# Kernel tuning notes

Measured on AMD Instinct MI355X. Metric: run time of the kernel, lower is better.

## Reference

```python
import jax, jax.numpy as jnp
import numpy as np

L, H, D, DH, FF, V, MAXPOS, SENSE, ATT = 12, 12, 768, 64, 3072, 30522, 512, 64, 64


def layer_norm(x, g, b, eps=1e-12):
    mu = jnp.mean(x, axis=-1, keepdims=True)
    var = jnp.mean((x - mu) ** 2, axis=-1, keepdims=True)
    return (x - mu) / jnp.sqrt(var + eps) * g + b


def setup_inputs() -> dict:
    key = jax.random.key(0)
    ks = jax.random.split(key, 24)
    B, S = 32, 256
    s = 0.02
    inp = {
        "input_ids": jax.random.randint(ks[0], (B, S), 0, V, dtype=jnp.int32),
        "token_type_ids": jnp.zeros((B, S), jnp.int32),
        "attention_mask": jnp.ones((B, S), jnp.int32),
        "location": jax.random.randint(ks[1], (B,), 1, S, dtype=jnp.int32),
        "sense_emb": jax.random.normal(ks[2], (SENSE, D), jnp.float32),
        # embedding tables
        "word_emb": s * jax.random.normal(ks[3], (V, D), jnp.float32),
        "pos_emb": s * jax.random.normal(ks[4], (MAXPOS, D), jnp.float32),
        "type_emb": s * jax.random.normal(ks[5], (2, D), jnp.float32),
        "emb_ln_g": jnp.ones((D,), jnp.float32),
        "emb_ln_b": jnp.zeros((D,), jnp.float32),
        # stacked per-layer transformer weights [L, ...]
        "Wq": s * jax.random.normal(ks[6], (L, D, D), jnp.float32),
        "bq": jnp.zeros((L, D), jnp.float32),
        "Wk": s * jax.random.normal(ks[7], (L, D, D), jnp.float32),
        "bk": jnp.zeros((L, D), jnp.float32),
        "Wv": s * jax.random.normal(ks[8], (L, D, D), jnp.float32),
        "bv": jnp.zeros((L, D), jnp.float32),
        "Wo": s * jax.random.normal(ks[9], (L, D, D), jnp.float32),
        "bo": jnp.zeros((L, D), jnp.float32),
        "ln1_g": jnp.ones((L, D), jnp.float32),
        "ln1_b": jnp.zeros((L, D), jnp.float32),
        "W1": s * jax.random.normal(ks[10], (L, D, FF), jnp.float32),
        "b1": jnp.zeros((L, FF), jnp.float32),
        "W2": s * jax.random.normal(ks[11], (L, FF, D), jnp.float32),
        "b2": jnp.zeros((L, D), jnp.float32),
        "ln2_g": jnp.ones((L, D), jnp.float32),
        "ln2_b": jnp.zeros((L, D), jnp.float32),
        # SelfAttention(sense_num) projections, scale dim = 64
        "att_Wq": s * jax.random.normal(ks[12], (D, ATT), jnp.float32),
        "att_Wk": s * jax.random.normal(ks[13], (D, ATT), jnp.float32),
    }
    return inp


def bert_encode(input_ids, token_type_ids, attention_mask, word_emb, pos_emb,
                type_emb, emb_ln_g, emb_ln_b, Wq, bq, Wk, bk, Wv, bv, Wo, bo,
                ln1_g, ln1_b, W1, b1, W2, b2, ln2_g, ln2_b):
    B, S = input_ids.shape
    x = word_emb[input_ids] + pos_emb[:S][None, :, :] + type_emb[token_type_ids]
    x = layer_norm(x, emb_ln_g, emb_ln_b)
    # additive mask bias: [B,1,1,S]
    bias = (1.0 - attention_mask.astype(x.dtype))[:, None, None, :] * -10000.0
    scale = 1.0 / jnp.sqrt(jnp.asarray(DH, x.dtype))
    for l in range(L):
        q = (x @ Wq[l] + bq[l]).reshape(B, S, H, DH).transpose(0, 2, 1, 3)
        k = (x @ Wk[l] + bk[l]).reshape(B, S, H, DH).transpose(0, 2, 1, 3)
        v = (x @ Wv[l] + bv[l]).reshape(B, S, H, DH).transpose(0, 2, 1, 3)
        scores = jnp.einsum("bhqd,bhkd->bhqk", q, k) * scale + bias
        attn = jax.nn.softmax(scores, axis=-1)
        o = jnp.einsum("bhqk,bhkd->bhqd", attn, v)
        o = o.transpose(0, 2, 1, 3).reshape(B, S, D)
        x = layer_norm(x + o @ Wo[l] + bo[l], ln1_g[l], ln1_b[l])
        h = jax.nn.gelu(x @ W1[l] + b1[l], approximate=False)
        x = layer_norm(x + h @ W2[l] + b2[l], ln2_g[l], ln2_b[l])
    return x


def reference(input_ids, token_type_ids, attention_mask, location, sense_emb,
              word_emb, pos_emb, type_emb, emb_ln_g, emb_ln_b, Wq, bq, Wk, bk,
              Wv, bv, Wo, bo, ln1_g, ln1_b, W1, b1, W2, b2, ln2_g, ln2_b,
              att_Wq, att_Wk):
    last_layer = bert_encode(input_ids, token_type_ids, attention_mask,
                             word_emb, pos_emb, type_emb, emb_ln_g, emb_ln_b,
                             Wq, bq, Wk, bk, Wv, bv, Wo, bo, ln1_g, ln1_b,
                             W1, b1, W2, b2, ln2_g, ln2_b)
    B = last_layer.shape[0]
    # gather the pun-word embedding at `location[i]` per row  -> [B, D]
    pun = last_layer[jnp.arange(B), location]
    # SelfAttention(sense_num) with scale 64: scaled dot-product scores [B, SENSE]
    scores = (pun @ att_Wq) @ (sense_emb @ att_Wk).T / jnp.sqrt(jnp.asarray(ATT, pun.dtype))
    res = jax.nn.softmax(scores, axis=1)
    # fused top-2 (replaces the original per-scalar Python loop)
    _, idx = jax.lax.top_k(res, 2)
    return idx.astype(jnp.float32)
```

## Files before the change

### kernel.cpp

```cpp
#include <hip/hip_runtime.h>
#include <math.h>

typedef __attribute__((ext_vector_type(8))) short short8;
typedef __attribute__((ext_vector_type(8))) _Float16 half8;
typedef __attribute__((ext_vector_type(4))) float f32x4;

static constexpr int Lc = 12;
static constexpr int Hc = 12;
static constexpr int Dc = 768;
static constexpr int DHc = 64;
static constexpr int FFc = 3072;
static constexpr int SENSEc = 64;
static constexpr int ATTc = 64;
static constexpr int QS = 3 * Dc;
static constexpr int KPAD = 72;

__device__ __forceinline__ unsigned short f2h(float f) {
    _Float16 h = (_Float16)f;
    union { _Float16 h; unsigned short u; } c;
    c.h = h;
    return c.u;
}

__device__ __forceinline__ void load_lds16(const void* g, void* l) {
    __builtin_amdgcn_global_load_lds(
        (const __attribute__((address_space(1))) unsigned int*)g,
        (__attribute__((address_space(3))) unsigned int*)l, 16, 0, 0);
}

__device__ __forceinline__ float blockReduceSum256(float v, float* sred) {
#pragma unroll
    for (int off = 32; off > 0; off >>= 1) v += __shfl_down(v, off, 64);
    int lane = threadIdx.x & 63, wid = threadIdx.x >> 6;
    if (lane == 0) sred[wid] = v;
    __syncthreads();
    float total = sred[0] + sred[1] + sred[2] + sred[3];
    __syncthreads();
    return total;
}

__global__ __launch_bounds__(256) void embed_kernel(
    const int* __restrict__ ids, const int* __restrict__ tts,
    const float* __restrict__ we, const float* __restrict__ pe,
    const float* __restrict__ te, const float* __restrict__ g,
    const float* __restrict__ b, float* __restrict__ x,
    unsigned short* __restrict__ xh, int S)
{
    int tok = blockIdx.x, t = threadIdx.x;
    int ss = tok % S;
    int id = ids[tok], tt = tts[tok];
    __shared__ float sred[4];
    float v[3];
    float s = 0.f;
#pragma unroll
    for (int i = 0; i < 3; ++i) {
        int d = t + i * 256;
        v[i] = we[(size_t)id * Dc + d] + pe[(size_t)ss * Dc + d] + te[(size_t)tt * Dc + d];
        s += v[i];
    }
    float mu = blockReduceSum256(s, sred) * (1.f / Dc);
    float s2 = 0.f;
#pragma unroll
    for (int i = 0; i < 3; ++i) { v[i] -= mu; s2 += v[i] * v[i]; }
    float rstd = rsqrtf(blockReduceSum256(s2, sred) * (1.f / Dc) + 1e-12f);
    size_t ro = (size_t)tok * Dc;
#pragma unroll
    for (int i = 0; i < 3; ++i) {
        int d = t + i * 256;
        float val = v[i] * rstd * g[d] + b[d];
        x[ro + d] = val;
        xh[ro + d] = f2h(val);
    }
}

__global__ __launch_bounds__(256) void resln_kernel(
    float* __restrict__ x, const float* __restrict__ y,
    const float* __restrict__ g, const float* __restrict__ b,
    unsigned short* __restrict__ xh)
{
    int tok = blockIdx.x, t = threadIdx.x;
    __shared__ float sred[4];
    size_t ro = (size_t)tok * Dc;
    float v[3];
    float s = 0.f;
#pragma unroll
    for (int i = 0; i < 3; ++i) {
        int d = t + i * 256;
        v[i] = x[ro + d] + y[ro + d];
        s += v[i];
    }
    float mu = blockReduceSum256(s, sred) * (1.f / Dc);
    float s2 = 0.f;
#pragma unroll
    for (int i = 0; i < 3; ++i) { v[i] -= mu; s2 += v[i] * v[i]; }
    float rstd = rsqrtf(blockReduceSum256(s2, sred) * (1.f / Dc) + 1e-12f);
#pragma unroll
    for (int i = 0; i < 3; ++i) {
        int d = t + i * 256;
        float val = v[i] * rstd * g[d] + b[d];
        x[ro + d] = val;
        xh[ro + d] = f2h(val);
    }
}

__global__ __launch_bounds__(256) void convert_weights(
    const float* __restrict__ Wq, const float* __restrict__ Wk,
    const float* __restrict__ Wv, const float* __restrict__ Wo,
    const float* __restrict__ W1, const float* __restrict__ W2,
    unsigned short* __restrict__ qh, unsigned short* __restrict__ oh,
    unsigned short* __restrict__ h1, unsigned short* __restrict__ h2)
{
    int id = blockIdx.x;
    const float* src; unsigned short *dh; int Kd, Nd, tx, ty;
    if (id < 576) {
        int m = id / 144, tile = id % 144;
        src = (m == 0) ? Wq : (m == 1) ? Wk : (m == 2) ? Wv : Wo;
        if (m < 3) { dh = qh + (size_t)m * Dc * Dc; }
        else       { dh = oh; }
        Kd = Dc; Nd = Dc; tx = tile % 12; ty = tile / 12;
    } else if (id < 1152) {
        int tile = id - 576;
        src = W1; dh = h1; Kd = Dc; Nd = FFc; tx = tile % 48; ty = tile / 48;
    } else {
        int tile = id - 1152;
        src = W2; dh = h2; Kd = FFc; Nd = Dc; tx = tile % 12; ty = tile / 12;
    }
    int k0 = ty * 64, n0 = tx * 64;
    __shared__ float tileS[64][65];
    int t = threadIdx.x, c = t & 63, r0 = t >> 6;
#pragma unroll
    for (int i = 0; i < 16; ++i) {
        int kr = r0 + i * 4;
        tileS[kr][c] = src[(size_t)(k0 + kr) * Nd + n0 + c];
    }
    __syncthreads();
#pragma unroll
    for (int i = 0; i < 16; ++i) {
        int nr = r0 + i * 4;
        float v = tileS[c][nr];
        size_t idx = (size_t)(n0 + nr) * Kd + k0 + c;
        dh[idx] = f2h(v);
    }
}

__global__ __launch_bounds__(256) void biascat_kernel(
    const float* __restrict__ bq, const float* __restrict__ bk,
    const float* __restrict__ bv, float* __restrict__ out)
{
    int lyr = blockIdx.x, t = threadIdx.x;
    for (int j = t; j < QS; j += 256) {
        float v = (j < Dc) ? bq[lyr * Dc + j]
                : (j < 2 * Dc) ? bk[lyr * Dc + j - Dc]
                : bv[lyr * Dc + j - 2 * Dc];
        out[lyr * QS + j] = v;
    }
}

template <int MODE>
__global__ __launch_bounds__(256, 3) void mfma_gemm_f16(
    const unsigned short* __restrict__ Ah, const unsigned short* __restrict__ Bh,
    const float* __restrict__ bias, float* __restrict__ Cf,
    unsigned short* __restrict__ Ch, int M, int N, int K)
{
    __shared__ alignas(16) unsigned short Ash[128 * 64];
    __shared__ alignas(16) unsigned short Bsh[128 * 64];
    int t = threadIdx.x, w = t >> 6, l = t & 63;
    int m0 = blockIdx.y * 128, n0 = blockIdx.x * 128;
    int wm = (w >> 1) * 64, wn = (w & 1) * 64;
    int sw = (((l & 7) ^ (l >> 3)) << 3);
    size_t go = (size_t)(w * 8 + (l >> 3)) * K + sw;
    const unsigned short* gah = Ah + (size_t)m0 * K + go;
    const unsigned short* gbh = Bh + (size_t)n0 * K + go;
    int lo = w * 512 + l * 8;
    f32x4 acc[4][4];
#pragma unroll
    for (int i = 0; i < 4; ++i)
#pragma unroll
        for (int j = 0; j < 4; ++j) acc[i][j] = (f32x4)0.f;
    int fm = l & 15, grp = l >> 4;
    int axor = fm & 7;
    for (int k0 = 0; k0 < K; k0 += 64) {
        __syncthreads();
#pragma unroll
        for (int i = 0; i < 4; ++i) {
            size_t g = (size_t)(i * 32) * K + k0;
            int d = lo + i * 2048;
            load_lds16(gah + g, Ash + d);
            load_lds16(gbh + g, Bsh + d);
        }
        __syncthreads();
#pragma unroll
        for (int h = 0; h < 2; ++h) {
            int koff = (((h * 4 + grp) ^ axor) << 3);
            half8 fa[4], fb[4];
#pragma unroll
            for (int i = 0; i < 4; ++i) {
                int ra = (wm + i * 16 + fm) * 64 + koff;
                int rb = (wn + i * 16 + fm) * 64 + koff;
                fa[i] = *(const half8*)(Ash + ra);
                fb[i] = *(const half8*)(Bsh + rb);
            }
#pragma unroll
            for (int i = 0; i < 4; ++i)
#pragma unroll
                for (int j = 0; j < 4; ++j)
                    acc[i][j] = __builtin_amdgcn_mfma_f32_16x16x32_f16(
                        fa[i], fb[j], acc[i][j], 0, 0, 0);
        }
    }
    int col_l = l & 15, row_l = (l >> 4) * 4;
#pragma unroll
    for (int j = 0; j < 4; ++j) {
        int col = n0 + wn + j * 16 + col_l;
        float bcv = bias[col];
#pragma unroll
        for (int i = 0; i < 4; ++i) {
            int row = m0 + wm + i * 16 + row_l;
#pragma unroll
            for (int r = 0; r < 4; ++r) {
                float v = acc[i][j][r] + bcv;
                size_t idx = (size_t)(row + r) * N + col;
                if (MODE == 1) {
                    v = 0.5f * v * (1.f + erff(v * 0.70710678118654752f));
                    Ch[idx] = f2h(v);
                } else if (MODE == 2) {
                    Ch[idx] = f2h(v);
                } else {
                    Cf[idx] = v;
                }
            }
        }
    }
}

__global__ __launch_bounds__(256, 1) void attn_mfma(
    const unsigned short* __restrict__ qkv, const int* __restrict__ mask,
    unsigned short* __restrict__ aoh, int B, int S)
{
    int bh = blockIdx.x, b = bh / Hc, hd = bh % Hc;
    int t = threadIdx.x, w = t >> 6, l = t & 63;
    int grp = l >> 4, lc = l & 15;
    __shared__ alignas(16) unsigned short Ks[256 * 64];
    __shared__ alignas(16) unsigned short Vts[4][64 * KPAD];
    __shared__ alignas(16) unsigned short Pw[4][64 * KPAD];
    __shared__ float mb[256];
    size_t rowbase = (size_t)(b * S) * QS;

    mb[t] = (1.f - (float)mask[b * S + t]) * -10000.0f;

    for (int p = 0; p < 4; ++p) {
        int key = p * 64 + (t >> 2);
        int d0 = (t & 3) * 16;
        const unsigned short* ksrc = qkv + rowbase + (size_t)key * QS + Dc + hd * DHc + d0;
        short8 s0 = *(const short8*)ksrc;
        short8 s1 = *(const short8*)(ksrc + 8);
        int c0 = d0 >> 3;
        *(short8*)(Ks + key * 64 + (((c0 + 0) ^ (key & 7)) << 3)) = s0;
        *(short8*)(Ks + key * 64 + (((c0 + 1) ^ (key & 7)) << 3)) = s1;
        const unsigned short* vsrc = qkv + rowbase + (size_t)key * QS + 2 * Dc + hd * DHc + d0;
        short8 v0 = *(const short8*)vsrc;
        short8 v1 = *(const short8*)(vsrc + 8);
        int kk = t >> 2;
#pragma unroll
        for (int u = 0; u < 8; ++u) {
            Vts[p][(d0 + u) * KPAD + kk]     = (unsigned short)v0[u];
            Vts[p][(d0 + 8 + u) * KPAD + kk] = (unsigned short)v1[u];
        }
    }

    int q0 = w * 64;
    half8 qf[4][2];
#pragma unroll
    for (int i = 0; i < 4; ++i)
#pragma unroll
        for (int kc = 0; kc < 2; ++kc)
            qf[i][kc] = *(const half8*)(qkv + rowbase
                        + (size_t)(q0 + 16 * i + lc) * QS + hd * DHc + kc * 32 + grp * 8);
    __syncthreads();

    f32x4 oacc[4][4];
#pragma unroll
    for (int i = 0; i < 4; ++i)
#pragma unroll
        for (int j = 0; j < 4; ++j) oacc[i][j] = (f32x4)0.f;
    float mstate[4][4], lstate[4][4];
#pragma unroll
    for (int i = 0; i < 4; ++i)
#pragma unroll
        for (int r = 0; r < 4; ++r) { mstate[i][r] = -3.0e38f; lstate[i][r] = 0.f; }

    for (int c = 0; c < 4; ++c) {
        f32x4 sacc[4][4];
#pragma unroll
        for (int i = 0; i < 4; ++i)
#pragma unroll
            for (int j = 0; j < 4; ++j) sacc[i][j] = (f32x4)0.f;
#pragma unroll
        for (int kc = 0; kc < 2; ++kc) {
            half8 kf[4];
#pragma unroll
            for (int j = 0; j < 4; ++j) {
                int krow = c * 64 + 16 * j + lc;
                kf[j] = *(const half8*)(Ks + krow * 64 + (((kc * 4 + grp) ^ (lc & 7)) << 3));
            }
#pragma unroll
            for (int i = 0; i < 4; ++i)
#pragma unroll
                for (int j = 0; j < 4; ++j)
                    sacc[i][j] = __builtin_amdgcn_mfma_f32_16x16x32_f16(
                        qf[i][kc], kf[j], sacc[i][j], 0, 0, 0);
        }
#pragma unroll
        for (int j = 0; j < 4; ++j) {
            float mbv = mb[c * 64 + 16 * j + lc];
#pragma unroll
            for (int i = 0; i < 4; ++i)
#pragma unroll
                for (int r = 0; r < 4; ++r)
                    sacc[i][j][r] = sacc[i][j][r] * 0.125f + mbv;
        }
#pragma unroll
        for (int i = 0; i < 4; ++i)
#pragma unroll
            for (int r = 0; r < 4; ++r) {
                float cm = fmaxf(fmaxf(sacc[i][0][r], sacc[i][1][r]),
                                 fmaxf(sacc[i][2][r], sacc[i][3][r]));
#pragma unroll
                for (int mw = 1; mw < 16; mw <<= 1)
                    cm = fmaxf(cm, __shfl_xor(cm, mw, 16));
                float nm = fmaxf(mstate[i][r], cm);
                float alpha = expf(mstate[i][r] - nm);
                mstate[i][r] = nm;
                float rs = 0.f;
#pragma unroll
                for (int j = 0; j < 4; ++j) {
                    float p = expf(sacc[i][j][r] - nm);
                    sacc[i][j][r] = p;
                    rs += p;
                }
#pragma unroll
                for (int mw = 1; mw < 16; mw <<= 1)
                    rs += __shfl_xor(rs, mw, 16);
                lstate[i][r] = lstate[i][r] * alpha + rs;
#pragma unroll
                for (int j = 0; j < 4; ++j) oacc[i][j][r] *= alpha;
            }
#pragma unroll
        for (int i = 0; i < 4; ++i)
#pragma unroll
            for (int j = 0; j < 4; ++j)
#pragma unroll
                for (int r = 0; r < 4; ++r)
                    Pw[w][(16 * i + 4 * grp + r) * KPAD + 16 * j + lc] =
                        f2h(sacc[i][j][r]);
        __syncthreads();
#pragma unroll
        for (int kc = 0; kc < 2; ++kc) {
            half8 pf[4], vf[4];
#pragma unroll
            for (int i = 0; i < 4; ++i)
                pf[i] = *(const half8*)(&Pw[w][(16 * i + lc) * KPAD + kc * 32 + grp * 8]);
#pragma unroll
            for (int j = 0; j < 4; ++j)
                vf[j] = *(const half8*)(&Vts[c][(16 * j + lc) * KPAD + kc * 32 + grp * 8]);
#pragma unroll
            for (int i = 0; i < 4; ++i)
#pragma unroll
                for (int j = 0; j < 4; ++j)
                    oacc[i][j] = __builtin_amdgcn_mfma_f32_16x16x32_f16(
                        pf[i], vf[j], oacc[i][j], 0, 0, 0);
        }
        __syncthreads();
    }
#pragma unroll
    for (int i = 0; i < 4; ++i)
#pragma unroll
        for (int r = 0; r < 4; ++r) {
            float inv = 1.f / lstate[i][r];
            size_t tok = (size_t)(b * S + q0 + 16 * i + 4 * grp + r);
#pragma unroll
            for (int j = 0; j < 4; ++j) {
                float v = oacc[i][j][r] * inv;
                size_t idx = tok * Dc + hd * DHc + 16 * j + lc;
                aoh[idx] = f2h(v);
            }
        }
}

__global__ __launch_bounds__(64) void pun_proj_kernel(
    const float* __restrict__ x, const int* __restrict__ loc,
    const float* __restrict__ Wq, float* __restrict__ pq, int S)
{
    __shared__ float pun[Dc];
    int b = blockIdx.x, t = threadIdx.x;
    const float* row = x + ((size_t)b * S + loc[b]) * Dc;
    for (int i = t; i < Dc; i += 64) pun[i] = row[i];
    __syncthreads();
    float acc = 0.f;
    for (int d = 0; d < Dc; ++d) acc += pun[d] * Wq[(size_t)d * ATTc + t];
    pq[b * ATTc + t] = acc;
}

__global__ __launch_bounds__(64) void sense_proj_kernel(
    const float* __restrict__ se, const float* __restrict__ Wk,
    float* __restrict__ sk)
{
    __shared__ float srow[Dc];
    int i = blockIdx.x, t = threadIdx.x;
    const float* row = se + (size_t)i * Dc;
    for (int j = t; j < Dc; j += 64) srow[j] = row[j];
    __syncthreads();
    float acc = 0.f;
    for (int d = 0; d < Dc; ++d) acc += srow[d] * Wk[(size_t)d * ATTc + t];
    sk[i * ATTc + t] = acc;
}

__global__ __launch_bounds__(64) void top2_kernel(
    const float* __restrict__ pq, const float* __restrict__ sk,
    float* __restrict__ out)
{
    __shared__ float pqs[ATTc];
    __shared__ float scs[SENSEc];
    int b = blockIdx.x, t = threadIdx.x;
    pqs[t] = pq[b * ATTc + t];
    __syncthreads();
    float acc = 0.f;
#pragma unroll
    for (int d = 0; d < ATTc; ++d) acc += pqs[d] * sk[t * ATTc + d];
    scs[t] = acc;
    __syncthreads();
    if (t == 0) {
        float v1 = -INFINITY, v2 = -INFINITY;
        int i1 = 0, i2 = 0;
        for (int i = 0; i < SENSEc; ++i) {
            float s = scs[i];
            if (s > v1) { v2 = v1; i2 = i1; v1 = s; i1 = i; }
            else if (s > v2) { v2 = s; i2 = i; }
        }
        out[b * 2 + 0] = (float)i1;
        out[b * 2 + 1] = (float)i2;
    }
}

extern "C" void kernel_launch(void* const* d_in, const int* in_sizes, int n_in,
                              void* d_out, int out_size, void* d_ws, size_t ws_size,
                              hipStream_t stream)
{
    (void)n_in; (void)out_size; (void)ws_size;
    const int*   input_ids  = (const int*)d_in[0];
    const int*   token_type = (const int*)d_in[1];
    const int*   attn_mask  = (const int*)d_in[2];
    const int*   location   = (const int*)d_in[3];
    const float* sense_emb  = (const float*)d_in[4];
    const float* word_emb   = (const float*)d_in[5];
    const float* pos_emb    = (const float*)d_in[6];
    const float* type_emb   = (const float*)d_in[7];
    const float* eg         = (const float*)d_in[8];
    const float* eb         = (const float*)d_in[9];
    const float* Wq         = (const float*)d_in[10];
    const float* bq         = (const float*)d_in[11];
    const float* Wk         = (const float*)d_in[12];
    const float* bk         = (const float*)d_in[13];
    const float* Wv         = (const float*)d_in[14];
    const float* bv         = (const float*)d_in[15];
    const float* Wo         = (const float*)d_in[16];
    const float* bo         = (const float*)d_in[17];
    const float* ln1g       = (const float*)d_in[18];
    const float* ln1b       = (const float*)d_in[19];
    const float* W1         = (const float*)d_in[20];
    const float* b1         = (const float*)d_in[21];
    const float* W2         = (const float*)d_in[22];
    const float* b2         = (const float*)d_in[23];
    const float* ln2g       = (const float*)d_in[24];
    const float* ln2b       = (const float*)d_in[25];
    const float* attWq      = (const float*)d_in[26];
    const float* attWk      = (const float*)d_in[27];
    float* out = (float*)d_out;

    int B = in_sizes[3];
    int S = in_sizes[0] / B;
    int NT = B * S;
    size_t NTD = (size_t)NT * Dc;

    float*          x   = (float*)d_ws;
    unsigned short* xh  = (unsigned short*)(x + NTD);
    float*          y   = (float*)(xh + NTD);
    unsigned short* hh  = (unsigned short*)(y + NTD);
    unsigned short* qkv = hh;
    unsigned short* aoh = qkv + (size_t)NT * QS;
    float*          bc  = (float*)(hh + (size_t)NT * FFc);
    unsigned short* wqh = (unsigned short*)(bc + (size_t)Lc * QS);
    unsigned short* woh = wqh + (size_t)QS * Dc;
    unsigned short* w1h = woh + (size_t)Dc * Dc;
    unsigned short* w2h = w1h + (size_t)FFc * Dc;
    float*          pq  = (float*)(w2h + (size_t)Dc * FFc);
    float*          sk  = pq + (size_t)B * ATTc;

    embed_kernel<<<NT, 256, 0, stream>>>(input_ids, token_type, word_emb,
                                         pos_emb, type_emb, eg, eb, x, xh, S);
    biascat_kernel<<<Lc, 256, 0, stream>>>(bq, bk, bv, bc);

    dim3 gQKV(QS / 128, NT / 128);
    dim3 gD(Dc / 128, NT / 128);
    dim3 gF(FFc / 128, NT / 128);
    for (int l = 0; l < Lc; ++l) {
        convert_weights<<<1728, 256, 0, stream>>>(
            Wq + (size_t)l * Dc * Dc, Wk + (size_t)l * Dc * Dc,
            Wv + (size_t)l * Dc * Dc, Wo + (size_t)l * Dc * Dc,
            W1 + (size_t)l * Dc * FFc, W2 + (size_t)l * FFc * Dc,
            wqh, woh, w1h, w2h);
        mfma_gemm_f16<2><<<gQKV, 256, 0, stream>>>(
            xh, wqh, bc + (size_t)l * QS, nullptr, qkv, NT, QS, Dc);
        attn_mfma<<<B * Hc, 256, 0, stream>>>(qkv, attn_mask, aoh, B, S);
        mfma_gemm_f16<0><<<gD, 256, 0, stream>>>(
            aoh, woh, bo + (size_t)l * Dc, y, nullptr, NT, Dc, Dc);
        resln_kernel<<<NT, 256, 0, stream>>>(x, y, ln1g + (size_t)l * Dc,
                                             ln1b + (size_t)l * Dc, xh);
        mfma_gemm_f16<1><<<gF, 256, 0, stream>>>(
            xh, w1h, b1 + (size_t)l * FFc, nullptr, hh, NT, FFc, Dc);
        mfma_gemm_f16<0><<<gD, 256, 0, stream>>>(
            hh, w2h, b2 + (size_t)l * Dc, y, nullptr, NT, Dc, FFc);
        resln_kernel<<<NT, 256, 0, stream>>>(x, y, ln2g + (size_t)l * Dc,
                                             ln2b + (size_t)l * Dc, xh);
    }

    pun_proj_kernel<<<B, 64, 0, stream>>>(x, location, attWq, pq, S);
    sense_proj_kernel<<<SENSEc, 64, 0, stream>>>(sense_emb, attWk, sk);
    top2_kernel<<<B, 64, 0, stream>>>(pq, sk, out);
}
```

Baseline: 3.768 ms.

## Double-buffer LDS tiles in MFMA GEMM to overlap global loads with compute

The GEMM kernel now keeps two LDS buffers for the A and B tiles. It issues the direct-to-LDS loads for the next K tile before computing on the current one, and uses a partial vmcnt wait so only the current tile's loads must have landed. This hides global load latency behind the MFMA work. In exchange, LDS use per block doubles to 64KB and the occupancy hint drops from 3 to 2 blocks per CU.

```diff
diff --git a/kernel.cpp b/kernel.cpp
--- a/kernel.cpp
+++ b/kernel.cpp
@@ -157,13 +157,13 @@
 }
 
 template <int MODE>
-__global__ __launch_bounds__(256, 3) void mfma_gemm_f16(
+__global__ __launch_bounds__(256, 2) void mfma_gemm_f16(
     const unsigned short* __restrict__ Ah, const unsigned short* __restrict__ Bh,
     const float* __restrict__ bias, float* __restrict__ Cf,
     unsigned short* __restrict__ Ch, int M, int N, int K)
 {
-    __shared__ alignas(16) unsigned short Ash[128 * 64];
-    __shared__ alignas(16) unsigned short Bsh[128 * 64];
+    __shared__ alignas(16) unsigned short Ash[2][128 * 64];
+    __shared__ alignas(16) unsigned short Bsh[2][128 * 64];
     int t = threadIdx.x, w = t >> 6, l = t & 63;
     int m0 = blockIdx.y * 128, n0 = blockIdx.x * 128;
     int wm = (w >> 1) * 64, wn = (w & 1) * 64;
@@ -179,16 +179,34 @@
         for (int j = 0; j < 4; ++j) acc[i][j] = (f32x4)0.f;
     int fm = l & 15, grp = l >> 4;
     int axor = fm & 7;
-    for (int k0 = 0; k0 < K; k0 += 64) {
-        __syncthreads();
-#pragma unroll
-        for (int i = 0; i < 4; ++i) {
-            size_t g = (size_t)(i * 32) * K + k0;
-            int d = lo + i * 2048;
-            load_lds16(gah + g, Ash + d);
-            load_lds16(gbh + g, Bsh + d);
-        }
-        __syncthreads();
+    int nk = K >> 6;
+
+#define STAGE_TILE(buf, k0)                                          \
+    {                                                                \
+        _Pragma("unroll")                                            \
+        for (int i = 0; i < 4; ++i) {                                \
+            size_t g = (size_t)(i * 32) * K + (k0);                  \
+            int d = lo + i * 2048;                                   \
+            load_lds16(gah + g, &Ash[buf][0] + d);                   \
+            load_lds16(gbh + g, &Bsh[buf][0] + d);                   \
+        }                                                            \
+    }
+
+    STAGE_TILE(0, 0);
+    int cur = 0;
+    for (int tk = 0; tk < nk; ++tk) {
+        __builtin_amdgcn_s_barrier();
+        __builtin_amdgcn_sched_barrier(0);
+        if (tk + 1 < nk) {
+            STAGE_TILE(cur ^ 1, (tk + 1) << 6);
+            asm volatile("s_waitcnt vmcnt(8)" ::: "memory");
+        } else {
+            asm volatile("s_waitcnt vmcnt(0)" ::: "memory");
+        }
+        __builtin_amdgcn_s_barrier();
+        __builtin_amdgcn_sched_barrier(0);
+        const unsigned short* As = &Ash[cur][0];
+        const unsigned short* Bs = &Bsh[cur][0];
 #pragma unroll
         for (int h = 0; h < 2; ++h) {
             int koff = (((h * 4 + grp) ^ axor) << 3);
@@ -197,8 +215,8 @@
             for (int i = 0; i < 4; ++i) {
                 int ra = (wm + i * 16 + fm) * 64 + koff;
                 int rb = (wn + i * 16 + fm) * 64 + koff;
-                fa[i] = *(const half8*)(Ash + ra);
-                fb[i] = *(const half8*)(Bsh + rb);
+                fa[i] = *(const half8*)(As + ra);
+                fb[i] = *(const half8*)(Bs + rb);
             }
 #pragma unroll
             for (int i = 0; i < 4; ++i)
@@ -207,7 +225,9 @@
                     acc[i][j] = __builtin_amdgcn_mfma_f32_16x16x32_f16(
                         fa[i], fb[j], acc[i][j], 0, 0, 0);
         }
-    }
+        cur ^= 1;
+    }
+#undef STAGE_TILE
     int col_l = l & 15, row_l = (l >> 4) * 4;
 #pragma unroll
     for (int j = 0; j < 4; ++j) {
```

New measurement: 4.031 ms. 1.07x slower.
